# Performance work log

Hardware: AMD Instinct MI355X
Metric: run time of the kernel (lower is better)

The kernel has to match this reference:

```python
import jax, jax.numpy as jnp
import numpy as np

EMBED_DIM = 1024
NUM_HEADS = 16
HEAD_DIM = EMBED_DIM // NUM_HEADS
B, S = 4, 2048


def setup_inputs() -> dict:
    key = jax.random.key(0)
    ks = jax.random.split(key, 11)
    d = EMBED_DIM
    s = 1.0 / np.sqrt(d)
    return {
        "query": jax.random.normal(ks[0], (B, S, d), jnp.float32),
        "key": jax.random.normal(ks[1], (B, S, d), jnp.float32),
        "value": jax.random.normal(ks[2], (B, S, d), jnp.float32),
        "Wq": jax.random.normal(ks[3], (d, d), jnp.float32) * s,
        "bq": jnp.zeros((d,), jnp.float32),
        "Wk": jax.random.normal(ks[4], (d, d), jnp.float32) * s,
        "bk": jnp.zeros((d,), jnp.float32),
        "Wv": jax.random.normal(ks[5], (d, d), jnp.float32) * s,
        "bv": jnp.zeros((d,), jnp.float32),
        "Wo": jax.random.normal(ks[6], (d, d), jnp.float32) * s,
        "bo": jnp.zeros((d,), jnp.float32),
    }


def reference(query, key, value, Wq, bq, Wk, bk, Wv, bv, Wo, bo):
    b, t, d = query.shape
    s = key.shape[1]
    h, hd = NUM_HEADS, HEAD_DIM
    # Linear projections (torch Linear: x @ W.T + b)
    q = (query @ Wq.T + bq).reshape(b, t, h, hd).transpose(0, 2, 1, 3)  # [B,H,T,hd]
    k = (key @ Wk.T + bk).reshape(b, s, h, hd).transpose(0, 2, 1, 3)    # [B,H,S,hd]
    v = (value @ Wv.T + bv).reshape(b, s, h, hd).transpose(0, 2, 1, 3)  # [B,H,S,hd]
    scale = 1.0 / np.sqrt(hd).astype(np.float32)
    attn = jnp.einsum('bhtd,bhsd->bhts', q, k) * scale  # [B,H,T,S]
    attn = jax.nn.softmax(attn, axis=-1)
    out = jnp.einsum('bhts,bhsd->bhtd', attn, v)        # [B,H,T,hd]
    out = out.transpose(0, 2, 1, 3).reshape(b, t, d)    # [B,T,D]
    out = out @ Wo.T + bo
    return out
```

## Files before the change

kernel.cpp:

```cpp
#include <hip/hip_runtime.h>
#include <hip/hip_bf16.h>
#include <stdint.h>

typedef __attribute__((ext_vector_type(8))) short short8;
typedef __attribute__((ext_vector_type(4))) float floatx4;
typedef __attribute__((ext_vector_type(16))) float floatx16;
typedef __attribute__((ext_vector_type(4))) uint16_t ushort4v;

#define MFMA16(a, b, c) __builtin_amdgcn_mfma_f32_16x16x32_bf16((a), (b), (c), 0, 0, 0)
#define MFMA32(a, b, c) __builtin_amdgcn_mfma_f32_32x32x16_bf16((a), (b), (c), 0, 0, 0)

#define GLOAD_LDS16(g, l)                                                          \
  __builtin_amdgcn_global_load_lds(                                                \
      (const __attribute__((address_space(1))) uint32_t*)(g),                      \
      (__attribute__((address_space(3))) uint32_t*)(l), 16, 0, 0)

#define CVTPK(lo_, hi_, out_) \
  asm("v_cvt_pk_bf16_f32 %0, %1, %2" : "=v"(out_) : "v"(lo_), "v"(hi_))
#define SWAP32(a_, b_) \
  asm("v_permlane32_swap_b32 %0, %1" : "+v"(a_), "+v"(b_))

__device__ __forceinline__ uint16_t f2bf(float x) {
  union { float f; uint32_t u; } c; c.f = x;
  return (uint16_t)((c.u + 0x7FFFu + ((c.u >> 16) & 1u)) >> 16);
}

__global__ void cvt3_k(const float* __restrict__ s0, const float* __restrict__ s1,
                       const float* __restrict__ s2, uint16_t* __restrict__ dst, int n4) {
  const float* src = blockIdx.z == 0 ? s0 : (blockIdx.z == 1 ? s1 : s2);
  uint16_t* d = dst + (size_t)blockIdx.z * 8388608;
  int stride = gridDim.x * blockDim.x;
  for (int i = blockIdx.x * blockDim.x + threadIdx.x; i < n4; i += stride) {
    float4 v = ((const float4*)src)[i];
    ushort4v o;
    o.x = f2bf(v.x); o.y = f2bf(v.y); o.z = f2bf(v.z); o.w = f2bf(v.w);
    ((ushort4v*)d)[i] = o;
  }
}
__global__ void cvt4_k(const float* __restrict__ s0, const float* __restrict__ s1,
                       const float* __restrict__ s2, const float* __restrict__ s3,
                       uint16_t* __restrict__ dst, int n4) {
  const float* src = blockIdx.z == 0 ? s0 : (blockIdx.z == 1 ? s1 : (blockIdx.z == 2 ? s2 : s3));
  uint16_t* d = dst + (size_t)blockIdx.z * 1048576;
  int stride = gridDim.x * blockDim.x;
  for (int i = blockIdx.x * blockDim.x + threadIdx.x; i < n4; i += stride) {
    float4 v = ((const float4*)src)[i];
    ushort4v o;
    o.x = f2bf(v.x); o.y = f2bf(v.y); o.z = f2bf(v.z); o.w = f2bf(v.w);
    ((ushort4v*)d)[i] = o;
  }
}

template <int MODE>
__device__ __forceinline__ void gemm_body(const uint16_t* __restrict__ A,
                                          const uint16_t* __restrict__ W,
                                          const float* __restrict__ bias,
                                          void* __restrict__ Cout, float scale,
                                          int brow, int bcol) {
  constexpr int N = 1024, K = 1024;
  __shared__ uint16_t As[32 * 128];
  __shared__ uint16_t Bs[32 * 128];
  const int t = threadIdx.x;
  const int l = t & 63;
  const int w = t >> 6;
  const int wr = w >> 1, wc = w & 1;
  const int l16 = l & 15, lhi = l >> 4;

  floatx4 acc[4][4] = {};

  for (int k0 = 0; k0 < K; k0 += 32) {
#pragma unroll
    for (int j = 0; j < 2; ++j) {
      int c = j * 256 + t;
      int r = c >> 4, qs = c & 15;
      int q0 = qs ^ (r & 15);
      int arow = 32 * (q0 >> 2) + r;
      int ko = (q0 & 3) * 8;
      const uint16_t* ga = A + (size_t)(brow + arow) * K + k0 + ko;
      const uint16_t* gb = W + (size_t)(bcol + arow) * K + k0 + ko;
      GLOAD_LDS16(ga, As + (size_t)(j * 256 + w * 64) * 8);
      GLOAD_LDS16(gb, Bs + (size_t)(j * 256 + w * 64) * 8);
    }
    __syncthreads();

    short8 a[4], b[4];
#pragma unroll
    for (int m = 0; m < 4; ++m) {
      int ar = wr * 64 + m * 16 + l16;
      a[m] = *(const short8*)&As[(ar & 31) * 128 + ((((ar >> 5) * 4 + lhi) ^ (ar & 15))) * 8];
    }
#pragma unroll
    for (int n = 0; n < 4; ++n) {
      int br_ = wc * 64 + n * 16 + l16;
      b[n] = *(const short8*)&Bs[(br_ & 31) * 128 + ((((br_ >> 5) * 4 + lhi) ^ (br_ & 15))) * 8];
    }
#pragma unroll
    for (int m = 0; m < 4; ++m)
#pragma unroll
      for (int n = 0; n < 4; ++n)
        acc[m][n] = MFMA16(a[m], b[n], acc[m][n]);
    __syncthreads();
  }

#pragma unroll
  for (int n = 0; n < 4; ++n) {
    int col = bcol + wc * 64 + n * 16 + l16;
    float bv = bias[col];
    if (MODE == 2) {
      int h = col >> 6, d = col & 63;
#pragma unroll
      for (int m = 0; m < 4; ++m) {
        int row = brow + wr * 64 + m * 16 + lhi * 4;
        int b_ = row >> 11, s = row & 2047;
        union { uint16_t u[4]; ushort4v v; } pk4;
#pragma unroll
        for (int j = 0; j < 4; ++j) pk4.u[j] = f2bf(acc[m][n][j] + bv);
        *(ushort4v*)((uint16_t*)Cout + (size_t)(b_ * 16 + h) * 131072 + (size_t)d * 2048 + s) = pk4.v;
      }
    } else {
#pragma unroll
      for (int m = 0; m < 4; ++m) {
#pragma unroll
        for (int j = 0; j < 4; ++j) {
          int row = brow + wr * 64 + m * 16 + lhi * 4 + j;
          float v = (acc[m][n][j] + bv) * scale;
          if (MODE == 1)
            ((uint16_t*)Cout)[(size_t)row * N + col] = f2bf(v);
          else
            ((float*)Cout)[(size_t)row * N + col] = v;
        }
      }
    }
  }
}

__global__ __launch_bounds__(256)
void gemm_qkv_k(const uint16_t* __restrict__ XQ, const uint16_t* __restrict__ XK,
                const uint16_t* __restrict__ XV, const uint16_t* __restrict__ WQ,
                const uint16_t* __restrict__ WK, const uint16_t* __restrict__ WV,
                const float* __restrict__ bq, const float* __restrict__ bk,
                const float* __restrict__ bv, uint16_t* __restrict__ QP,
                uint16_t* __restrict__ KP, uint16_t* __restrict__ VT, float qscale) {
  const int f = (blockIdx.z * 64 + blockIdx.y) * 8 + blockIdx.x;
  const int virt = (f & 7) * 192 + (f >> 3);
  const int vz = virt >> 9;
  const int vy = (virt & 511) >> 3;
  const int vx = virt & 7;

  if (vz == 0)      gemm_body<1>(XQ, WQ, bq, QP, qscale, vy * 128, vx * 128);
  else if (vz == 1) gemm_body<1>(XK, WK, bk, KP, 1.0f,  vy * 128, vx * 128);
  else              gemm_body<2>(XV, WV, bv, VT, 1.0f,  vy * 128, vx * 128);
}

__global__ __launch_bounds__(256)
void gemm_o_k(const uint16_t* __restrict__ A, const uint16_t* __restrict__ W,
              const float* __restrict__ bias, float* __restrict__ Cout) {
  const int f = blockIdx.y * 8 + blockIdx.x;
  const int virt = (f & 7) * 64 + (f >> 3);
  const int vy = virt >> 3;
  const int vx = virt & 7;
  gemm_body<0>(A, W, bias, Cout, 1.0f, vy * 128, vx * 128);
}

__global__ __launch_bounds__(512, 2)
void attn_k(const uint16_t* __restrict__ Qp, const uint16_t* __restrict__ Kp,
            const uint16_t* __restrict__ Vt, uint16_t* __restrict__ AO) {
  __shared__ uint16_t Kl[2][64 * 128];
  __shared__ uint16_t Vl[2][64 * 128];

  const int t = threadIdx.x;
  const int l = t & 63, w = t >> 6;
  const int l32 = l & 31, hi = l >> 5;

  const int f = blockIdx.y * 8 + blockIdx.x;
  const int virt = (f & 7) * 64 + (f >> 3);
  const int vx = virt & 7;
  const int vy = virt >> 3;

  const int q0 = vx * 256 + w * 32;
  const size_t base = (size_t)(vy >> 4) * 2048 * 1024 + (size_t)(vy & 15) * 64;
  const size_t vbg = (size_t)vy * 131072;

  union PAu { uint32_t u[4]; short8 s; };

  const uint16_t* pK[2];
  const uint16_t* pV[2];
#pragma unroll
  for (int i = 0; i < 2; ++i) {
    int c = i * 512 + t;
    int r = c >> 4, qs = c & 15;
    int q0c = qs ^ (r & 15);
    pK[i] = Kp + base + (size_t)(64 * (q0c >> 3) + r) * 1024 + (q0c & 7) * 8;
    pV[i] = Vt + vbg + (size_t)r * 2048 + q0c * 8;
  }

#define STAGE_ALL(NB)                                                 \
  {                                                                   \
    _Pragma("unroll") for (int i = 0; i < 2; ++i) {                   \
      GLOAD_LDS16(pK[i], &Kl[NB][(size_t)(i * 512 + w * 64) * 8]);    \
      GLOAD_LDS16(pV[i], &Vl[NB][(size_t)(i * 512 + w * 64) * 8]);    \
      pK[i] += 131072;                          \
      pV[i] += 128;                             \
    }                                                                 \
  }

  short8 qf[4];
#pragma unroll
  for (int ks = 0; ks < 4; ++ks)
    qf[ks] = *(const short8*)(Qp + base + (size_t)(q0 + l32) * 1024 + ks * 16 + hi * 8);

  floatx16 of0 = {}, of1 = {};
  float rs = 0.f;

  const int swzb = (l32 & 15);
  const int krow = l32 * 256;

  STAGE_ALL(0);
  __syncthreads();

#define QK_Q(SF, CUR, H, RH)                                                          \
  {                                                                                   \
    _Pragma("unroll") for (int ks = 0; ks < 4; ++ks) {                                \
      int kbyte = krow + (RH) * 8192 + ((((H) * 8 + 2 * ks + hi) ^ swzb) << 4);       \
      short8 kf = *(const short8*)((char*)Kl[CUR] + kbyte);                           \
      SF = MFMA32(kf, qf[ks], SF);                                                    \
    }                                                                                 \
  }

#define EXPPACK(SF, P0, P1)                                                           \
  {                                                                                   \
    _Pragma("unroll") for (int r = 0; r < 16; ++r) {                                  \
      SF[r] = __builtin_amdgcn_exp2f(SF[r]);                                          \
      rs += SF[r];                                                                    \
    }                                                                                 \
    uint32_t a0, a1, b0, b1;                                                          \
    CVTPK(SF[0], SF[1], a0); CVTPK(SF[2], SF[3], a1);                                 \
    CVTPK(SF[4], SF[5], b0); CVTPK(SF[6], SF[7], b1);                                 \
    SWAP32(a0, b0); SWAP32(a1, b1);                                                   \
    P0.u[0] = a0; P0.u[1] = a1; P0.u[2] = b0; P0.u[3] = b1;                           \
    CVTPK(SF[8], SF[9], a0); CVTPK(SF[10], SF[11], a1);                               \
    CVTPK(SF[12], SF[13], b0); CVTPK(SF[14], SF[15], b1);                             \
    SWAP32(a0, b0); SWAP32(a1, b1);                                                   \
    P1.u[0] = a0; P1.u[1] = a1; P1.u[2] = b0; P1.u[3] = b1;                           \
  }

#define PV_Q(P0, P1, CUR, H, RH)                                                      \
  {                                                                                   \
    int vb0 = krow + ((((H) * 8 + 2 * (2 * (RH)) + hi) ^ swzb) << 4);                 \
    int vb1 = krow + ((((H) * 8 + 2 * (2 * (RH) + 1) + hi) ^ swzb) << 4);             \
    short8 vf00 = *(const short8*)((char*)Vl[CUR] + vb0);                             \
    short8 vf01 = *(const short8*)((char*)Vl[CUR] + vb0 + 8192);                      \
    short8 vf10 = *(const short8*)((char*)Vl[CUR] + vb1);                             \
    short8 vf11 = *(const short8*)((char*)Vl[CUR] + vb1 + 8192);                      \
    of0 = MFMA32(P0.s, vf00, of0);                                                    \
    of1 = MFMA32(P0.s, vf01, of1);                                                    \
    of0 = MFMA32(P1.s, vf10, of0);                                                    \
    of1 = MFMA32(P1.s, vf11, of1);                                                    \
  }

#define STEP128(CUR, PF)                                                              \
  {                                                                                   \
    if (PF) STAGE_ALL(CUR ^ 1);                                                       \
    floatx16 sfA = {}, sfB = {};                                                      \
    QK_Q(sfA, CUR, 0, 0);                                                             \
    QK_Q(sfB, CUR, 0, 1);                                                             \
    {                                                                                 \
      PAu p0, p1;                                                                     \
      EXPPACK(sfA, p0, p1);                                                           \
      PV_Q(p0, p1, CUR, 0, 0);                                                        \
    }                                                                                 \
    sfA = (floatx16){};                                                               \
    QK_Q(sfA, CUR, 1, 0);                                                             \
    {                                                                                 \
      PAu p0, p1;                                                                     \
      EXPPACK(sfB, p0, p1);                                                           \
      PV_Q(p0, p1, CUR, 0, 1);                                                        \
    }                                                                                 \
    sfB = (floatx16){};                                                               \
    QK_Q(sfB, CUR, 1, 1);                                                             \
    {                                                                                 \
      PAu p0, p1;                                                                     \
      EXPPACK(sfA, p0, p1);                                                           \
      PV_Q(p0, p1, CUR, 1, 0);                                                        \
    }                                                                                 \
    {                                                                                 \
      PAu p0, p1;                                                                     \
      EXPPACK(sfB, p0, p1);                                                           \
      PV_Q(p0, p1, CUR, 1, 1);                                                        \
    }                                                                                 \
    __syncthreads();                                                                  \
  }

  for (int it = 0; it < 8; ++it) {
    STEP128(0, 1);
    STEP128(1, it < 7);
  }

  rs += __shfl_xor(rs, 32);
#pragma unroll
  for (int r = 0; r < 16; ++r) {
    int qloc = (r & 3) + 8 * (r >> 2) + 4 * hi;
    float rsq = __shfl(rs, qloc);
    float rinv = 1.0f / rsq;
    int qrow = q0 + qloc;
    AO[base + (size_t)qrow * 1024 + l32]      = f2bf(of0[r] * rinv);
    AO[base + (size_t)qrow * 1024 + 32 + l32] = f2bf(of1[r] * rinv);
  }
#undef STAGE_ALL
#undef QK_Q
#undef EXPPACK
#undef PV_Q
#undef STEP128
}

extern "C" void kernel_launch(void* const* d_in, const int* in_sizes, int n_in,
                              void* d_out, int out_size, void* d_ws, size_t ws_size,
                              hipStream_t stream) {
  const float* q  = (const float*)d_in[0];
  const float* k  = (const float*)d_in[1];
  const float* v  = (const float*)d_in[2];
  const float* Wq = (const float*)d_in[3];
  const float* bq = (const float*)d_in[4];
  const float* Wk = (const float*)d_in[5];
  const float* bk = (const float*)d_in[6];
  const float* Wv = (const float*)d_in[7];
  const float* bv = (const float*)d_in[8];
  const float* Wo = (const float*)d_in[9];
  const float* bo = (const float*)d_in[10];

  const size_t MB = 1ull << 20;
  char* ws = (char*)d_ws;
  uint16_t* XQ  = (uint16_t*)(ws + 0 * MB);
  uint16_t* XK  = (uint16_t*)(ws + 16 * MB);
  uint16_t* XV  = (uint16_t*)(ws + 32 * MB);
  uint16_t* WQb = (uint16_t*)(ws + 48 * MB);
  uint16_t* WKb = (uint16_t*)(ws + 50 * MB);
  uint16_t* WVb = (uint16_t*)(ws + 52 * MB);
  uint16_t* WOb = (uint16_t*)(ws + 54 * MB);
  uint16_t* QP  = (uint16_t*)(ws + 56 * MB);
  uint16_t* KP  = (uint16_t*)(ws + 72 * MB);
  uint16_t* VT  = (uint16_t*)(ws + 88 * MB);
  uint16_t* AO  = XQ;

  const int NTOK = 4 * 2048;
  const int D = 1024;
  const int nBig = NTOK * D / 4;
  const int nW = D * D / 4;
  const float qscale = 0.125f * 1.4426950408889634f;

  cvt3_k<<<dim3(2048, 1, 3), dim3(256), 0, stream>>>(q, k, v, XQ, nBig);
  cvt4_k<<<dim3(1024, 1, 4), dim3(256), 0, stream>>>(Wq, Wk, Wv, Wo, WQb, nW);

  gemm_qkv_k<<<dim3(D / 128, NTOK / 128, 3), dim3(256), 0, stream>>>(
      XQ, XK, XV, WQb, WKb, WVb, bq, bk, bv, QP, KP, VT, qscale);

  attn_k<<<dim3(8, 64), dim3(512), 0, stream>>>(QP, KP, VT, AO);

  gemm_o_k<<<dim3(D / 128, NTOK / 128), dim3(256), 0, stream>>>(AO, WOb, bo, (float*)d_out);
}
```

Baseline: 196.5 us.

## Rewrite projection GEMMs with 256x128 tiles, BK=64 and triple-buffered LDS pipeline

Replaces the 128x128, BK=32 single-buffered GEMM body with a 256x128 tile run by 512 threads, 64-wide K steps and a three-stage LDS ring. Global-to-LDS loads for the next stages are issued before computing the current one, with explicit vmcnt waits and one barrier per step instead of two. The aim is to hide load latency and cut barrier overhead in the QKV and output projections. In exchange it needs more LDS per block (about 144 KB), which limits occupancy to one block per CU, and it halves the grid size, which may leave some CUs idle.

```diff
diff --git a/kernel.cpp b/kernel.cpp
--- a/kernel.cpp
+++ b/kernel.cpp
@@ -19,6 +19,17 @@
   asm("v_cvt_pk_bf16_f32 %0, %1, %2" : "=v"(out_) : "v"(lo_), "v"(hi_))
 #define SWAP32(a_, b_) \
   asm("v_permlane32_swap_b32 %0, %1" : "+v"(a_), "+v"(b_))
+
+#define WAITVM(N)                                          \
+  {                                                        \
+    asm volatile("s_waitcnt vmcnt(" #N ")" ::: "memory");  \
+    __builtin_amdgcn_sched_barrier(0);                     \
+  }
+#define SBAR                                               \
+  {                                                        \
+    __builtin_amdgcn_s_barrier();                          \
+    __builtin_amdgcn_sched_barrier(0);                     \
+  }
 
 __device__ __forceinline__ uint16_t f2bf(float x) {
   union { float f; uint32_t u; } c; c.f = x;
@@ -52,65 +63,103 @@
 }
 
 template <int MODE>
-__device__ __forceinline__ void gemm_body(const uint16_t* __restrict__ A,
-                                          const uint16_t* __restrict__ W,
-                                          const float* __restrict__ bias,
-                                          void* __restrict__ Cout, float scale,
-                                          int brow, int bcol) {
+__device__ __forceinline__ void gemm256_body(uint16_t* __restrict__ As,
+                                             uint16_t* __restrict__ Bs,
+                                             const uint16_t* __restrict__ A,
+                                             const uint16_t* __restrict__ W,
+                                             const float* __restrict__ bias,
+                                             void* __restrict__ Cout, float scale,
+                                             int brow, int bcol) {
   constexpr int N = 1024, K = 1024;
-  __shared__ uint16_t As[32 * 128];
-  __shared__ uint16_t Bs[32 * 128];
   const int t = threadIdx.x;
-  const int l = t & 63;
-  const int w = t >> 6;
-  const int wr = w >> 1, wc = w & 1;
-  const int l16 = l & 15, lhi = l >> 4;
+  const int l = t & 63, w = t >> 6;
+  const int l16 = l & 15, lhi = (l >> 4) & 3;
+  const int wm = w >> 1, wn = w & 1;
+
+  const uint16_t* pA[4];
+  const uint16_t* pB[2];
+#pragma unroll
+  for (int i = 0; i < 4; ++i) {
+    int cw = (i * 512 + t) & 1023;
+    int r = cw >> 4, q = cw & 15;
+    int q0 = q ^ (r & 15);
+    pA[i] = A + (size_t)(brow + (i >> 1) * 128 + 64 * (q0 >> 3) + r) * K + (q0 & 7) * 8;
+  }
+#pragma unroll
+  for (int i = 0; i < 2; ++i) {
+    int c = i * 512 + t;
+    int r = c >> 4, q = c & 15;
+    int q0 = q ^ (r & 15);
+    pB[i] = W + (size_t)(bcol + 64 * (q0 >> 3) + r) * K + (q0 & 7) * 8;
+  }
+
+#define G_STAGE(BUF)                                                      \
+  {                                                                       \
+    _Pragma("unroll") for (int i = 0; i < 4; ++i) {                       \
+      GLOAD_LDS16(pA[i], As + (BUF) * 16384 + i * 4096 + w * 512);        \
+      pA[i] += 64;                                                        \
+    }                                                                     \
+    _Pragma("unroll") for (int i = 0; i < 2; ++i) {                       \
+      GLOAD_LDS16(pB[i], Bs + (BUF) * 8192 + i * 4096 + w * 512);         \
+      pB[i] += 64;                                                        \
+    }                                                                     \
+  }
 
   floatx4 acc[4][4] = {};
 
-  for (int k0 = 0; k0 < K; k0 += 32) {
-#pragma unroll
-    for (int j = 0; j < 2; ++j) {
-      int c = j * 256 + t;
-      int r = c >> 4, qs = c & 15;
-      int q0 = qs ^ (r & 15);
-      int arow = 32 * (q0 >> 2) + r;
-      int ko = (q0 & 3) * 8;
-      const uint16_t* ga = A + (size_t)(brow + arow) * K + k0 + ko;
-      const uint16_t* gb = W + (size_t)(bcol + arow) * K + k0 + ko;
-      GLOAD_LDS16(ga, As + (size_t)(j * 256 + w * 64) * 8);
-      GLOAD_LDS16(gb, Bs + (size_t)(j * 256 + w * 64) * 8);
-    }
-    __syncthreads();
-
-    short8 a[4], b[4];
-#pragma unroll
-    for (int m = 0; m < 4; ++m) {
-      int ar = wr * 64 + m * 16 + l16;
-      a[m] = *(const short8*)&As[(ar & 31) * 128 + ((((ar >> 5) * 4 + lhi) ^ (ar & 15))) * 8];
-    }
-#pragma unroll
-    for (int n = 0; n < 4; ++n) {
-      int br_ = wc * 64 + n * 16 + l16;
-      b[n] = *(const short8*)&Bs[(br_ & 31) * 128 + ((((br_ >> 5) * 4 + lhi) ^ (br_ & 15))) * 8];
-    }
-#pragma unroll
-    for (int m = 0; m < 4; ++m)
-#pragma unroll
-      for (int n = 0; n < 4; ++n)
-        acc[m][n] = MFMA16(a[m], b[n], acc[m][n]);
-    __syncthreads();
-  }
+#define G_COMPUTE(BUF)                                                               \
+  {                                                                                  \
+    short8 a[4][2], b[4][2];                                                         \
+    _Pragma("unroll") for (int m = 0; m < 4; ++m)                                    \
+      _Pragma("unroll") for (int ks = 0; ks < 2; ++ks)                               \
+        a[m][ks] = *(const short8*)((const char*)(As + (BUF) * 16384) +              \
+            (wm >> 1) * 16384 +                                                      \
+            (m * 16 + l16) * 256 + ((((wm & 1) * 8 + ks * 4 + lhi) ^ l16) << 4));    \
+    _Pragma("unroll") for (int n = 0; n < 4; ++n)                                    \
+      _Pragma("unroll") for (int ks = 0; ks < 2; ++ks)                               \
+        b[n][ks] = *(const short8*)((const char*)(Bs + (BUF) * 8192) +               \
+            (n * 16 + l16) * 256 + (((wn * 8 + ks * 4 + lhi) ^ l16) << 4));          \
+    _Pragma("unroll") for (int ks = 0; ks < 2; ++ks)                                 \
+      _Pragma("unroll") for (int m = 0; m < 4; ++m)                                  \
+        _Pragma("unroll") for (int n = 0; n < 4; ++n)                                \
+          acc[m][n] = MFMA16(a[m][ks], b[n][ks], acc[m][n]);                         \
+  }
+
+#define G_STEP(RD, ST)   \
+  {                      \
+    G_STAGE(ST);         \
+    G_COMPUTE(RD);       \
+    WAITVM(6);           \
+    SBAR;                \
+  }
+
+  G_STAGE(0);
+  G_STAGE(1);
+  WAITVM(6);
+  SBAR;
+
+#pragma unroll 1
+  for (int g = 0; g < 4; ++g) {
+    G_STEP(0, 2);
+    G_STEP(1, 0);
+    G_STEP(2, 1);
+  }
+  G_STEP(0, 2);
+  G_STEP(1, 0);
+  G_COMPUTE(2);
+  WAITVM(0);
+  SBAR;
+  G_COMPUTE(0);
 
 #pragma unroll
   for (int n = 0; n < 4; ++n) {
-    int col = bcol + wc * 64 + n * 16 + l16;
+    int col = bcol + wn * 64 + n * 16 + l16;
     float bv = bias[col];
     if (MODE == 2) {
       int h = col >> 6, d = col & 63;
 #pragma unroll
       for (int m = 0; m < 4; ++m) {
-        int row = brow + wr * 64 + m * 16 + lhi * 4;
+        int row = brow + wm * 64 + m * 16 + lhi * 4;
         int b_ = row >> 11, s = row & 2047;
         union { uint16_t u[4]; ushort4v v; } pk4;
 #pragma unroll
@@ -122,7 +171,7 @@
       for (int m = 0; m < 4; ++m) {
 #pragma unroll
         for (int j = 0; j < 4; ++j) {
-          int row = brow + wr * 64 + m * 16 + lhi * 4 + j;
+          int row = brow + wm * 64 + m * 16 + lhi * 4 + j;
           float v = (acc[m][n][j] + bv) * scale;
           if (MODE == 1)
             ((uint16_t*)Cout)[(size_t)row * N + col] = f2bf(v);
@@ -132,34 +181,40 @@
       }
     }
   }
-}
-
-__global__ __launch_bounds__(256)
+#undef G_STAGE
+#undef G_COMPUTE
+#undef G_STEP
+}
+
+__global__ __launch_bounds__(512, 1)
 void gemm_qkv_k(const uint16_t* __restrict__ XQ, const uint16_t* __restrict__ XK,
                 const uint16_t* __restrict__ XV, const uint16_t* __restrict__ WQ,
                 const uint16_t* __restrict__ WK, const uint16_t* __restrict__ WV,
                 const float* __restrict__ bq, const float* __restrict__ bk,
                 const float* __restrict__ bv, uint16_t* __restrict__ QP,
                 uint16_t* __restrict__ KP, uint16_t* __restrict__ VT, float qscale) {
-  const int f = (blockIdx.z * 64 + blockIdx.y) * 8 + blockIdx.x;
-  const int virt = (f & 7) * 192 + (f >> 3);
-  const int vz = virt >> 9;
-  const int vy = (virt & 511) >> 3;
-  const int vx = virt & 7;
-
-  if (vz == 0)      gemm_body<1>(XQ, WQ, bq, QP, qscale, vy * 128, vx * 128);
-  else if (vz == 1) gemm_body<1>(XK, WK, bk, KP, 1.0f,  vy * 128, vx * 128);
-  else              gemm_body<2>(XV, WV, bv, VT, 1.0f,  vy * 128, vx * 128);
-}
-
-__global__ __launch_bounds__(256)
+  __shared__ uint16_t As[3 * 16384];
+  __shared__ uint16_t Bs[3 * 8192];
+  const int f = (blockIdx.z * 32 + blockIdx.y) * 8 + blockIdx.x;
+  const int virt = (f & 7) * 96 + (f >> 3);
+  const int vz = virt >> 8;
+  const int rem = virt & 255;
+  const int vy = rem >> 3, vx = rem & 7;
+
+  if (vz == 0)      gemm256_body<1>(As, Bs, XQ, WQ, bq, QP, qscale, vy * 256, vx * 128);
+  else if (vz == 1) gemm256_body<1>(As, Bs, XK, WK, bk, KP, 1.0f,  vy * 256, vx * 128);
+  else              gemm256_body<2>(As, Bs, XV, WV, bv, VT, 1.0f,  vy * 256, vx * 128);
+}
+
+__global__ __launch_bounds__(512, 1)
 void gemm_o_k(const uint16_t* __restrict__ A, const uint16_t* __restrict__ W,
               const float* __restrict__ bias, float* __restrict__ Cout) {
+  __shared__ uint16_t As[3 * 16384];
+  __shared__ uint16_t Bs[3 * 8192];
   const int f = blockIdx.y * 8 + blockIdx.x;
-  const int virt = (f & 7) * 64 + (f >> 3);
-  const int vy = virt >> 3;
-  const int vx = virt & 7;
-  gemm_body<0>(A, W, bias, Cout, 1.0f, vy * 128, vx * 128);
+  const int virt = (f & 7) * 32 + (f >> 3);
+  const int vy = virt >> 3, vx = virt & 7;
+  gemm256_body<0>(As, Bs, A, W, bias, Cout, 1.0f, vy * 256, vx * 128);
 }
 
 __global__ __launch_bounds__(512, 2)
@@ -351,10 +406,10 @@
   cvt3_k<<<dim3(2048, 1, 3), dim3(256), 0, stream>>>(q, k, v, XQ, nBig);
   cvt4_k<<<dim3(1024, 1, 4), dim3(256), 0, stream>>>(Wq, Wk, Wv, Wo, WQb, nW);
 
-  gemm_qkv_k<<<dim3(D / 128, NTOK / 128, 3), dim3(256), 0, stream>>>(
+  gemm_qkv_k<<<dim3(8, 32, 3), dim3(512), 0, stream>>>(
       XQ, XK, XV, WQb, WKb, WVb, bq, bk, bv, QP, KP, VT, qscale);
 
   attn_k<<<dim3(8, 64), dim3(512), 0, stream>>>(QP, KP, VT, AO);
 
-  gemm_o_k<<<dim3(D / 128, NTOK / 128), dim3(256), 0, stream>>>(AO, WOb, bo, (float*)d_out);
-}
+  gemm_o_k<<<dim3(8, 32), dim3(512), 0, stream>>>(AO, WOb, bo, (float*)d_out);
+}
```

After: 185.7 us. 5.5% less time.
